# Kernel tuning notes

Hardware: AMD Instinct MI355X
Metric: run time of the kernel (lower is better)

## Reference

```python
import jax, jax.numpy as jnp
import numpy as np

DIM, NH, WS, SR, CTS = 256, 8, 8, 4, 2
HD = DIM // NH
SCALE = HD ** -0.5

def _linear(x, w, b=None):
    y = x @ w.T
    return y + b if b is not None else y

def _ln(x, g, b, eps=1e-5):
    m = jnp.mean(x, -1, keepdims=True)
    v = jnp.mean((x - m) ** 2, -1, keepdims=True)
    return (x - m) / jnp.sqrt(v + eps) * g + b

def _mlp(x, w1, b1, w2, b2):
    return _linear(jax.nn.gelu(_linear(x, w1, b1), approximate=False), w2, b2)

def _pos_emb_rank3(seq_len, w1, b1, w2):
    # PosEmbMLPSwinv1D with rank=3: coords on cube_root(seq) grid, normalized
    s = int(round(seq_len ** (1.0 / 3.0)))
    c = (jnp.arange(s, dtype=jnp.float32) - s // 2) / (s // 2)
    grid = jnp.stack(jnp.meshgrid(c, c, c, indexing='ij'))      # (3,s,s,s)
    tbl = grid.reshape(3, -1).T                                 # (s^3,3)
    return _linear(jax.nn.relu(_linear(tbl, w1, b1)), w2)[None]  # (1,s^3,dim)

def _rel_bias_3d(ws, w1, b1, w2, n_global):
    # PosEmbMLPSwinv3D: CPB-MLP bias over 3D relative coords, 16*sigmoid, zero-pad for carrier tokens
    r = jnp.arange(-(ws - 1), ws, dtype=jnp.float32)
    tbl = jnp.stack(jnp.meshgrid(r, r, r, indexing='ij'), axis=-1) / (ws - 1)
    tbl = tbl * 8.0
    tbl = jnp.sign(tbl) * jnp.log2(jnp.abs(tbl) + 1.0) / np.log2(8.0)
    table = _linear(jax.nn.relu(_linear(tbl.reshape(-1, 3), w1, b1)), w2)  # ((2ws-1)^3, NH)
    coords = jnp.stack(jnp.meshgrid(jnp.arange(ws), jnp.arange(ws), jnp.arange(ws), indexing='ij'))
    cf = coords.reshape(3, -1)
    rel = (cf[:, :, None] - cf[:, None, :]).transpose(1, 2, 0) + (ws - 1)  # (P,P,3)
    idx = rel[..., 0] * (2 * ws - 1) ** 2 + rel[..., 1] * (2 * ws - 1) + rel[..., 2]
    P = ws ** 3
    bias = table[idx.reshape(-1)].reshape(P, P, NH).transpose(2, 0, 1)
    bias = 16.0 * jax.nn.sigmoid(bias)
    return jnp.pad(bias, ((0, 0), (n_global, 0), (n_global, 0)))[None]  # (1,NH,P+g,P+g)

def _win_attn(x, qkv_w, qkv_b, proj_w, proj_b, bias):
    B, N, C = x.shape
    qkv = _linear(x, qkv_w, qkv_b).reshape(B, N, 3, NH, HD).transpose(2, 0, 3, 1, 4)
    q, k, v = qkv[0], qkv[1], qkv[2]
    attn = jax.nn.softmax(jnp.einsum('bhnd,bhmd->bhnm', q, k) * SCALE + bias, axis=-1)
    out = jnp.einsum('bhnm,bhmd->bhnd', attn, v).transpose(0, 2, 1, 3).reshape(B, N, C)
    return _linear(out, proj_w, proj_b)

def _ct_dewindow(ct, W, H, D, ws):
    bs, _, N = ct.shape
    c = ct.reshape(bs, W // ws, H // ws, D // ws, ws, ws, ws, N)
    c = c.transpose(0, 7, 1, 3, 5, 2, 4, 6).reshape(bs, N, W * H * D)
    return c.transpose(0, 2, 1)

def _ct_window(ct, W, H, D, ws):
    bs, _, N = ct.shape
    c = ct.reshape(bs, H // ws, ws, W // ws, ws, D // ws, ws, N)
    return c.transpose(0, 1, 3, 5, 2, 4, 6, 7)

def setup_inputs() -> dict:
    key = jax.random.key(0)
    ks = jax.random.split(key, 48)
    B0 = 1
    nw = SR ** 3
    def w(k, *s):
        return jax.random.normal(k, s, jnp.float32) * 0.02
    def b(k, *s):
        return jax.random.normal(k, s, jnp.float32) * 0.01
    d4 = 4 * DIM
    return {
        'x': jax.random.normal(ks[0], (B0 * nw, WS ** 3, DIM), jnp.float32),
        'ct': jax.random.normal(ks[1], (B0, (CTS * SR) ** 3, DIM), jnp.float32),
        'pe_w1': w(ks[2], 512, 3), 'pe_b1': b(ks[3], 512), 'pe_w2': w(ks[4], DIM, 512),
        'hpe_w1': w(ks[5], 512, 3), 'hpe_b1': b(ks[6], 512), 'hpe_w2': w(ks[7], DIM, 512),
        'hat_n1_g': jnp.ones((DIM,), jnp.float32), 'hat_n1_b': jnp.zeros((DIM,), jnp.float32),
        'hat_qkv_w': w(ks[8], 3 * DIM, DIM), 'hat_qkv_b': b(ks[9], 3 * DIM),
        'hat_proj_w': w(ks[10], DIM, DIM), 'hat_proj_b': b(ks[11], DIM),
        'hat_cpb_w1': w(ks[12], 512, 3), 'hat_cpb_b1': b(ks[13], 512), 'hat_cpb_w2': w(ks[14], NH, 512),
        'hat_n2_g': jnp.ones((DIM,), jnp.float32), 'hat_n2_b': jnp.zeros((DIM,), jnp.float32),
        'hat_fc1_w': w(ks[15], d4, DIM), 'hat_fc1_b': b(ks[16], d4),
        'hat_fc2_w': w(ks[17], DIM, d4), 'hat_fc2_b': b(ks[18], DIM),
        'n1_g': jnp.ones((DIM,), jnp.float32), 'n1_b': jnp.zeros((DIM,), jnp.float32),
        'qkv_w': w(ks[19], 3 * DIM, DIM), 'qkv_b': b(ks[20], 3 * DIM),
        'proj_w': w(ks[21], DIM, DIM), 'proj_b': b(ks[22], DIM),
        'cpb_w1': w(ks[23], 512, 3), 'cpb_b1': b(ks[24], 512), 'cpb_w2': w(ks[25], NH, 512),
        'n2_g': jnp.ones((DIM,), jnp.float32), 'n2_b': jnp.zeros((DIM,), jnp.float32),
        'fc1_w': w(ks[26], d4, DIM), 'fc1_b': b(ks[27], d4),
        'fc2_w': w(ks[28], DIM, d4), 'fc2_b': b(ks[29], DIM),
    }

def reference(x, ct, pe_w1, pe_b1, pe_w2, hpe_w1, hpe_b1, hpe_w2,
              hat_n1_g, hat_n1_b, hat_qkv_w, hat_qkv_b, hat_proj_w, hat_proj_b,
              hat_cpb_w1, hat_cpb_b1, hat_cpb_w2, hat_n2_g, hat_n2_b,
              hat_fc1_w, hat_fc1_b, hat_fc2_w, hat_fc2_b,
              n1_g, n1_b, qkv_w, qkv_b, proj_w, proj_b,
              cpb_w1, cpb_b1, cpb_w2, n2_g, n2_b, fc1_w, fc1_b, fc2_w, fc2_b):
    Bg, Ng, Hg = ct.shape
    G = CTS * SR  # carrier-token global cube side
    x = x + _pos_emb_rank3(x.shape[1], pe_w1, pe_b1, pe_w2)
    # carrier-token global attention (hierarchical path)
    ct = _ct_dewindow(ct, G, G, G, CTS)
    ct = ct + _pos_emb_rank3(ct.shape[1], hpe_w1, hpe_b1, hpe_w2)
    hat_bias = _rel_bias_3d(G, hat_cpb_w1, hat_cpb_b1, hat_cpb_w2, 0)
    ct = ct + _win_attn(_ln(ct, hat_n1_g, hat_n1_b), hat_qkv_w, hat_qkv_b, hat_proj_w, hat_proj_b, hat_bias)
    ct = ct + _mlp(_ln(ct, hat_n2_g, hat_n2_b), hat_fc1_w, hat_fc1_b, hat_fc2_w, hat_fc2_b)
    ct_w = _ct_window(ct, G, G, G, CTS).reshape(x.shape[0], -1, Hg)
    # windowed attention over [carrier tokens ; window tokens]
    x = jnp.concatenate([ct_w, x], axis=1)
    bias = _rel_bias_3d(WS, cpb_w1, cpb_b1, cpb_w2, CTS ** 3)
    x = x + _win_attn(_ln(x, n1_g, n1_b), qkv_w, qkv_b, proj_w, proj_b, bias)
    x = x + _mlp(_ln(x, n2_g, n2_b), fc1_w, fc1_b, fc2_w, fc2_b)
    split = x.shape[1] - WS ** 3
    ctr, x = x[:, :split], x[:, split:]
    return x, ctr.reshape(Bg, Ng, Hg)
```

## Files before the change

kernel.cpp:

```cpp
#include <hip/hip_runtime.h>
#include <hip/hip_bf16.h>
#include <math.h>

typedef __hip_bfloat16 bf16;

#define SCALE_QK 0.17677669529663687f

__device__ __forceinline__ float b2f(bf16 v){ return __bfloat162float(v); }
__device__ __forceinline__ bf16  f2b(float v){ return __float2bfloat16(v); }
__device__ __forceinline__ short bfs(float x){ bf16 b = f2b(x); short s; __builtin_memcpy(&s, &b, 2); return s; }

struct __align__(16) bf16x8 { bf16 v[8]; };
struct __align__(8)  bf16x4 { bf16 v[4]; };

typedef __attribute__((ext_vector_type(8))) short sh8;
typedef __attribute__((ext_vector_type(4))) short sh4;
typedef __attribute__((ext_vector_type(4))) float f4;

#if defined(__has_builtin)
#if __has_builtin(__builtin_amdgcn_mfma_f32_16x16x16bf16_1k)
#define HAS_MFMA16 1
#else
#define HAS_MFMA16 0
#endif
#else
#define HAS_MFMA16 0
#endif

#if defined(__has_builtin)
#if __has_builtin(__builtin_amdgcn_exp2f)
#define EXP2(x) __builtin_amdgcn_exp2f(x)
#else
#define EXP2(x) exp2f(x)
#endif
#else
#define EXP2(x) exp2f(x)
#endif

__global__ __launch_bounds__(256) void wcvt10_k(const float* s0, const float* s1, const float* s2, const float* s3,
                                                const float* s4, const float* s5, const float* s6, const float* s7,
                                                const float* s8, const float* s9,
                                                bf16* d0, bf16* d1, bf16* d2, bf16* d3, bf16* d4,
                                                bf16* d5, bf16* d6, bf16* d7, bf16* d8, bf16* d9) {
    const int sizes[10] = {196608, 65536, 262144, 262144, 196608, 65536, 262144, 262144, 131072, 131072};
    int which = blockIdx.y;
    const float* s; bf16* d;
    switch (which) {
        case 0: s = s0; d = d0; break;  case 1: s = s1; d = d1; break;
        case 2: s = s2; d = d2; break;  case 3: s = s3; d = d3; break;
        case 4: s = s4; d = d4; break;  case 5: s = s5; d = d5; break;
        case 6: s = s6; d = d6; break;  case 7: s = s7; d = d7; break;
        case 8: s = s8; d = d8; break;  default: s = s9; d = d9; break;
    }
    int i = blockIdx.x * 256 + threadIdx.x;
    if (i < sizes[which]) d[i] = f2b(s[i]);
}

__global__ __launch_bounds__(256) void hidbuild_k(const float* __restrict__ w1a, const float* __restrict__ b1a,
                                                  const float* __restrict__ w1b, const float* __restrict__ b1b,
                                                  bf16* __restrict__ hidA, bf16* __restrict__ hidB) {
    const float* w1 = blockIdx.y ? w1b : w1a;
    const float* b1 = blockIdx.y ? b1b : b1a;
    bf16* hid       = blockIdx.y ? hidB : hidA;
    int t = blockIdx.x, tid = threadIdx.x;
    int i = t >> 6, j = (t >> 3) & 7, k = t & 7;
    float c0 = (i - 4) * 0.25f, c1 = (j - 4) * 0.25f, c2 = (k - 4) * 0.25f;
    #pragma unroll
    for (int rep = 0; rep < 2; rep++) {
        int jj = tid + rep * 256;
        float h = c0 * w1[jj*3+0] + c1 * w1[jj*3+1] + c2 * w1[jj*3+2] + b1[jj];
        hid[(size_t)t * 512 + jj] = f2b(fmaxf(h, 0.f));
    }
}

__device__ __forceinline__ float cpb_coord(int idx) {
    float v = (idx - 7) * (8.0f / 7.0f);
    return copysignf(log2f(fabsf(v) + 1.0f) * (1.0f / 3.0f), v);
}
__global__ __launch_bounds__(512) void cpbtab_k(const float* __restrict__ w1a, const float* __restrict__ b1a,
                                                const float* __restrict__ w2a, float* __restrict__ taba,
                                                const float* __restrict__ w1b, const float* __restrict__ b1b,
                                                const float* __restrict__ w2b, float* __restrict__ tabb) {
    const float* w1 = blockIdx.y ? w1b : w1a;
    const float* b1 = blockIdx.y ? b1b : b1a;
    const float* w2 = blockIdx.y ? w2b : w2a;
    float* tab      = blockIdx.y ? tabb : taba;
    int t = blockIdx.x, tid = threadIdx.x;
    __shared__ float hid[512];
    int i = t / 225, r = t - i * 225, j = r / 15, k = r - j * 15;
    float x0 = cpb_coord(i), x1 = cpb_coord(j), x2 = cpb_coord(k);
    float h = x0 * w1[tid*3+0] + x1 * w1[tid*3+1] + x2 * w1[tid*3+2] + b1[tid];
    hid[tid] = fmaxf(h, 0.f);
    __syncthreads();
    int h8 = tid >> 6, lane = tid & 63;
    float p = 0.f;
    for (int jj = lane; jj < 512; jj += 64) p += hid[jj] * w2[h8*512 + jj];
    for (int off = 32; off; off >>= 1) p += __shfl_down(p, off);
    if (lane == 0) tab[t * 8 + h8] = p;
}

__global__ __launch_bounds__(256) void biasbuild_k(const float* __restrict__ taba, float* __restrict__ biasQa,
                                                   const float* __restrict__ tabb, float* __restrict__ biasQb) {
    const float* tab = blockIdx.y ? tabb : taba;
    float* biasQ     = blockIdx.y ? biasQb : biasQa;
    int idx = blockIdx.x * 256 + threadIdx.x;
    int h = idx >> 18, rem = idx & 262143;
    int q = rem >> 9, k = rem & 511;
    int qx = q >> 6, qy = (q >> 3) & 7, qz = q & 7;
    int kx = k >> 6, ky = (k >> 3) & 7, kz = k & 7;
    int tidx = ((qx - kx + 7) * 15 + (qy - ky + 7)) * 15 + (qz - kz + 7);
    float v = tab[tidx * 8 + h];
    float b = 16.f / (1.f + __expf(-v));
    biasQ[idx] = (b - 24.0f) * 1.4426950408889634f;
}

__global__ __launch_bounds__(256) void ct0build_k(const float* __restrict__ ct_in,
                                                  const float* __restrict__ hpe,
                                                  float* __restrict__ ct0) {
    int u = blockIdx.x, c = threadIdx.x;
    int a = u >> 7, cc = (u >> 5) & 3, e = (u >> 4) & 1, b = (u >> 2) & 3, d = (u >> 1) & 1, f = u & 1;
    int t = a * 128 + b * 32 + cc * 8 + d * 4 + e * 2 + f;
    ct0[(size_t)u * 256 + c] = ct_in[(size_t)t * 256 + c] + hpe[(size_t)u * 256 + c];
}

__global__ __launch_bounds__(256) void ln_k(const float* __restrict__ in,
                                            const float* __restrict__ g,
                                            const float* __restrict__ b,
                                            bf16* __restrict__ out) {
    int row = blockIdx.x, c = threadIdx.x;
    float x = in[(size_t)row * 256 + c];
    float s = x, s2 = x * x;
    for (int off = 32; off; off >>= 1) { s += __shfl_down(s, off); s2 += __shfl_down(s2, off); }
    __shared__ float red[8];
    int wid = c >> 6, lane = c & 63;
    if (lane == 0) { red[wid] = s; red[wid + 4] = s2; }
    __syncthreads();
    if (c == 0) { red[0] = red[0] + red[1] + red[2] + red[3]; red[4] = red[4] + red[5] + red[6] + red[7]; }
    __syncthreads();
    float mean = red[0] * (1.f / 256.f);
    float var  = fmaxf(red[4] * (1.f / 256.f) - mean * mean, 0.f);
    float rstd = rsqrtf(var + 1e-5f);
    out[(size_t)row * 256 + c] = f2b((x - mean) * rstd * g[c] + b[c]);
}

template <int MODE>
__global__ __launch_bounds__(256) void gemm_k(const bf16* __restrict__ A,
                                              const bf16* __restrict__ W,
                                              const float* __restrict__ bias,
                                              int M, int N, int K,
                                              float* __restrict__ res,
                                              bf16* __restrict__ outb) {
    __shared__ short As[128 * 40];
    __shared__ short Ws[128 * 40];
    int m0 = blockIdx.y * 128, n0 = blockIdx.x * 128;
    int tid = threadIdx.x;
    int lane = tid & 63, wave = tid >> 6;
    int quad = lane >> 4, m16 = lane & 15;
    int wm = (wave & 1) * 64, wn = (wave >> 1) * 64;
    int arow = tid >> 2, acol = (tid & 3) * 8;

    f4 acc[4][4];
    #pragma unroll
    for (int i = 0; i < 4; i++)
        #pragma unroll
        for (int j = 0; j < 4; j++) acc[i][j] = (f4){0.f, 0.f, 0.f, 0.f};

    for (int k0 = 0; k0 < K; k0 += 32) {
        sh8 a0 = *reinterpret_cast<const sh8*>(A + (size_t)(m0 + arow) * K + k0 + acol);
        sh8 a1 = *reinterpret_cast<const sh8*>(A + (size_t)(m0 + arow + 64) * K + k0 + acol);
        sh8 w0 = *reinterpret_cast<const sh8*>(W + (size_t)(n0 + arow) * K + k0 + acol);
        sh8 w1 = *reinterpret_cast<const sh8*>(W + (size_t)(n0 + arow + 64) * K + k0 + acol);
        __syncthreads();
        *reinterpret_cast<sh8*>(&As[arow * 40 + acol])        = a0;
        *reinterpret_cast<sh8*>(&As[(arow + 64) * 40 + acol]) = a1;
        *reinterpret_cast<sh8*>(&Ws[arow * 40 + acol])        = w0;
        *reinterpret_cast<sh8*>(&Ws[(arow + 64) * 40 + acol]) = w1;
        __syncthreads();
        sh8 af[4], bf[4];
        #pragma unroll
        for (int mi = 0; mi < 4; mi++)
            af[mi] = *reinterpret_cast<const sh8*>(&As[(wm + mi * 16 + m16) * 40 + quad * 8]);
        #pragma unroll
        for (int ni = 0; ni < 4; ni++)
            bf[ni] = *reinterpret_cast<const sh8*>(&Ws[(wn + ni * 16 + m16) * 40 + quad * 8]);
        #pragma unroll
        for (int mi = 0; mi < 4; mi++)
            #pragma unroll
            for (int ni = 0; ni < 4; ni++)
                acc[mi][ni] = __builtin_amdgcn_mfma_f32_16x16x32_bf16(af[mi], bf[ni], acc[mi][ni], 0, 0, 0);
    }
    (void)M;

    #pragma unroll
    for (int mi = 0; mi < 4; mi++) {
        #pragma unroll
        for (int r = 0; r < 4; r++) {
            int gm = m0 + wm + mi * 16 + quad * 4 + r;
            #pragma unroll
            for (int ni = 0; ni < 4; ni++) {
                int gn = n0 + wn + ni * 16 + m16;
                float v = acc[mi][ni][r];
                if constexpr (MODE != 3) v += bias[gn];
                if constexpr (MODE == 2)      res[(size_t)gm * N + gn] += v;
                else if constexpr (MODE == 3) res[(size_t)gm * N + gn] = v;
                else if constexpr (MODE == 1) outb[(size_t)gm * N + gn] = f2b(0.5f * v * (1.0f + erff(v * 0.70710678118654752f)));
                else                          outb[(size_t)gm * N + gn] = f2b(v);
            }
        }
    }
}

#define VSTR 548
#define SC2   0.25503575360579045f
#define CNB  (-34.62468098133512f)
#define NEGB (-1.0e30f)
__global__ __launch_bounds__(512) void flash_k(const bf16* __restrict__ qkv,
                                               const float* __restrict__ biasQ,
                                               bf16* __restrict__ out,
                                               int N, int glob) {
    int wh = blockIdx.x, w = wh >> 3, h = wh & 7;
    int qs = blockIdx.y, QS = gridDim.y;
    int tid = threadIdx.x;
    int lane = tid & 63, wave = tid >> 6;
    int quad = lane >> 4, qcol = lane & 15;
    const int NT32 = (N + 31) & ~31;

    __shared__ bf16 Vt[32 * VSTR];
#if !HAS_MFMA16
    __shared__ float Ps[8][16 * 17];
#endif

    for (int i = tid; i < NT32 * 4; i += 512) {
        int tok = i >> 2, seg = i & 3;
        if (tok < N) {
            const bf16* vp = qkv + ((size_t)(w * N + tok)) * 768 + 512 + h * 32 + seg * 8;
            bf16x8 vv = *reinterpret_cast<const bf16x8*>(vp);
            #pragma unroll
            for (int e = 0; e < 8; e++) Vt[(seg * 8 + e) * VSTR + tok] = vv.v[e];
        } else {
            bf16 z = f2b(0.f);
            #pragma unroll
            for (int e = 0; e < 8; e++) Vt[(seg * 8 + e) * VSTR + tok] = z;
        }
    }
    __syncthreads();

    const bf16* qbase = qkv + ((size_t)w * N) * 768 + h * 32;
    const bf16* kbase = qbase + 256;
    int nqt = (N + 15) >> 4, nkt = NT32 >> 5;
    int nun = (nqt + 1) >> 1;

    for (int u = wave * QS + qs; u < nun; u += 8 * QS) {
        bool hasB = (2 * u + 1 < nqt);
        int qA = u * 32 + qcol;
        int qB = qA + 16;
        int qrA = (qA < N) ? qA : (N - 1);
        int qrB = (qB < N) ? qB : (N - 1);
        sh8 qfA = *reinterpret_cast<const sh8*>(qbase + (size_t)qrA * 768 + quad * 8);
        sh8 qfB = *reinterpret_cast<const sh8*>(qbase + (size_t)qrB * 768 + quad * 8);
        f4 O0A = {0.f,0.f,0.f,0.f}, O1A = {0.f,0.f,0.f,0.f};
        f4 O0B = {0.f,0.f,0.f,0.f}, O1B = {0.f,0.f,0.f,0.f};
        float lA = 0.f, lB = 0.f;
        bool vA = (qA >= glob) && (qA < N);
        bool vB = (qB >= glob) && (qB < N);
        const float* browA = biasQ + (((size_t)h << 9) + (size_t)(vA ? (qA - glob) : 0)) * 512 - glob;
        const float* browB = biasQ + (((size_t)h << 9) + (size_t)(vB ? (qB - glob) : 0)) * 512 - glob;

        sh8 kf0, kf1;
        {
            int k0 = qcol, k1 = 16 + qcol;
            kf0 = *reinterpret_cast<const sh8*>(kbase + (size_t)((k0 < N) ? k0 : (N - 1)) * 768 + quad * 8);
            kf1 = *reinterpret_cast<const sh8*>(kbase + (size_t)((k1 < N) ? k1 : (N - 1)) * 768 + quad * 8);
        }

        for (int kt = 0; kt < nkt; kt++) {
            int bt = kt * 32;
            sh8 c0 = kf0, c1 = kf1;
            if (kt + 1 < nkt) {
                int n0 = bt + 32 + qcol, n1 = bt + 48 + qcol;
                kf0 = *reinterpret_cast<const sh8*>(kbase + (size_t)((n0 < N) ? n0 : (N - 1)) * 768 + quad * 8);
                kf1 = *reinterpret_cast<const sh8*>(kbase + (size_t)((n1 < N) ? n1 : (N - 1)) * 768 + quad * 8);
            }
            f4 z = {0.f, 0.f, 0.f, 0.f};
            f4 s0A = __builtin_amdgcn_mfma_f32_16x16x32_bf16(c0, qfA, z, 0, 0, 0);
            f4 s1A = __builtin_amdgcn_mfma_f32_16x16x32_bf16(c1, qfA, z, 0, 0, 0);
            f4 s0B = z, s1B = z;
            if (hasB) {
                s0B = __builtin_amdgcn_mfma_f32_16x16x32_bf16(c0, qfB, z, 0, 0, 0);
                s1B = __builtin_amdgcn_mfma_f32_16x16x32_bf16(c1, qfB, z, 0, 0, 0);
            }

            int tg0 = bt + quad * 4, tg1 = bt + 16 + quad * 4;
            bool val0 = tg0 < N, val1 = tg1 < N;
            f4 bb0A, bb1A;
            if (!val0)                    bb0A = (f4){NEGB, NEGB, NEGB, NEGB};
            else if (vA && tg0 >= glob)   bb0A = *reinterpret_cast<const f4*>(browA + tg0);
            else                          bb0A = (f4){CNB, CNB, CNB, CNB};
            if (!val1)                    bb1A = (f4){NEGB, NEGB, NEGB, NEGB};
            else if (vA && tg1 >= glob)   bb1A = *reinterpret_cast<const f4*>(browA + tg1);
            else                          bb1A = (f4){CNB, CNB, CNB, CNB};

            float pA[8];
            #pragma unroll
            for (int r = 0; r < 4; r++) {
                pA[r]     = EXP2(fmaf(s0A[r], SC2, bb0A[r]));
                pA[4 + r] = EXP2(fmaf(s1A[r], SC2, bb1A[r]));
            }
            #pragma unroll
            for (int r = 0; r < 8; r++) lA += pA[r];

            float pB[8];
            if (hasB) {
                f4 bb0B, bb1B;
                if (!val0)                    bb0B = (f4){NEGB, NEGB, NEGB, NEGB};
                else if (vB && tg0 >= glob)   bb0B = *reinterpret_cast<const f4*>(browB + tg0);
                else                          bb0B = (f4){CNB, CNB, CNB, CNB};
                if (!val1)                    bb1B = (f4){NEGB, NEGB, NEGB, NEGB};
                else if (vB && tg1 >= glob)   bb1B = *reinterpret_cast<const f4*>(browB + tg1);
                else                          bb1B = (f4){CNB, CNB, CNB, CNB};
                #pragma unroll
                for (int r = 0; r < 4; r++) {
                    pB[r]     = EXP2(fmaf(s0B[r], SC2, bb0B[r]));
                    pB[4 + r] = EXP2(fmaf(s1B[r], SC2, bb1B[r]));
                }
                #pragma unroll
                for (int r = 0; r < 8; r++) lB += pB[r];
            }

#if HAS_MFMA16
            sh4 v00 = *reinterpret_cast<const sh4*>(&Vt[qcol * VSTR + bt + quad * 4]);
            sh4 v10 = *reinterpret_cast<const sh4*>(&Vt[qcol * VSTR + bt + 16 + quad * 4]);
            sh4 v01 = *reinterpret_cast<const sh4*>(&Vt[(qcol + 16) * VSTR + bt + quad * 4]);
            sh4 v11 = *reinterpret_cast<const sh4*>(&Vt[(qcol + 16) * VSTR + bt + 16 + quad * 4]);
            sh4 pf0A, pf1A;
            #pragma unroll
            for (int r = 0; r < 4; r++) { pf0A[r] = bfs(pA[r]); pf1A[r] = bfs(pA[4 + r]); }
            O0A = __builtin_amdgcn_mfma_f32_16x16x16bf16_1k(v00, pf0A, O0A, 0, 0, 0);
            O0A = __builtin_amdgcn_mfma_f32_16x16x16bf16_1k(v10, pf1A, O0A, 0, 0, 0);
            O1A = __builtin_amdgcn_mfma_f32_16x16x16bf16_1k(v01, pf0A, O1A, 0, 0, 0);
            O1A = __builtin_amdgcn_mfma_f32_16x16x16bf16_1k(v11, pf1A, O1A, 0, 0, 0);
            if (hasB) {
                sh4 pf0B, pf1B;
                #pragma unroll
                for (int r = 0; r < 4; r++) { pf0B[r] = bfs(pB[r]); pf1B[r] = bfs(pB[4 + r]); }
                O0B = __builtin_amdgcn_mfma_f32_16x16x16bf16_1k(v00, pf0B, O0B, 0, 0, 0);
                O0B = __builtin_amdgcn_mfma_f32_16x16x16bf16_1k(v10, pf1B, O0B, 0, 0, 0);
                O1B = __builtin_amdgcn_mfma_f32_16x16x16bf16_1k(v01, pf0B, O1B, 0, 0, 0);
                O1B = __builtin_amdgcn_mfma_f32_16x16x16bf16_1k(v11, pf1B, O1B, 0, 0, 0);
            }
#else
            for (int t = 0; t < 2; t++) {
                if (t == 1 && !hasB) break;
                const float* ph = t ? pB : pA;
                for (int half = 0; half < 2; half++) {
                    #pragma unroll
                    for (int r = 0; r < 4; r++) Ps[wave][(quad * 4 + r) * 17 + qcol] = ph[half * 4 + r];
                    __builtin_amdgcn_wave_barrier();
                    sh8 pbig, va, vb;
                    #pragma unroll
                    for (int j = 0; j < 8; j++) {
                        int tl = quad * 8 + j;
                        float pv = (quad < 2) ? Ps[wave][tl * 17 + qcol] : 0.f;
                        pbig[j] = bfs(pv);
                        bf16 a0 = (quad < 2) ? Vt[qcol * VSTR + bt + half * 16 + tl] : f2b(0.f);
                        bf16 a1 = (quad < 2) ? Vt[(qcol + 16) * VSTR + bt + half * 16 + tl] : f2b(0.f);
                        short t0, t1;
                        __builtin_memcpy(&t0, &a0, 2); __builtin_memcpy(&t1, &a1, 2);
                        va[j] = t0; vb[j] = t1;
                    }
                    if (t == 0) {
                        O0A = __builtin_amdgcn_mfma_f32_16x16x32_bf16(va, pbig, O0A, 0, 0, 0);
                        O1A = __builtin_amdgcn_mfma_f32_16x16x32_bf16(vb, pbig, O1A, 0, 0, 0);
                    } else {
                        O0B = __builtin_amdgcn_mfma_f32_16x16x32_bf16(va, pbig, O0B, 0, 0, 0);
                        O1B = __builtin_amdgcn_mfma_f32_16x16x32_bf16(vb, pbig, O1B, 0, 0, 0);
                    }
                    __builtin_amdgcn_wave_barrier();
                }
            }
#endif
        }

        lA += __shfl_xor(lA, 16); lA += __shfl_xor(lA, 32);
        float rlA = 1.f / lA;
        if (qA < N) {
            bf16x4 o0, o1;
            #pragma unroll
            for (int r = 0; r < 4; r++) { o0.v[r] = f2b(O0A[r] * rlA); o1.v[r] = f2b(O1A[r] * rlA); }
            bf16* op = out + ((size_t)(w * N + qA)) * 256 + h * 32 + quad * 4;
            *reinterpret_cast<bf16x4*>(op)      = o0;
            *reinterpret_cast<bf16x4*>(op + 16) = o1;
        }
        if (hasB) {
            lB += __shfl_xor(lB, 16); lB += __shfl_xor(lB, 32);
            float rlB = 1.f / lB;
            if (qB < N) {
                bf16x4 o0, o1;
                #pragma unroll
                for (int r = 0; r < 4; r++) { o0.v[r] = f2b(O0B[r] * rlB); o1.v[r] = f2b(O1B[r] * rlB); }
                bf16* op = out + ((size_t)(w * N + qB)) * 256 + h * 32 + quad * 4;
                *reinterpret_cast<bf16x4*>(op)      = o0;
                *reinterpret_cast<bf16x4*>(op + 16) = o1;
            }
        }
    }
}

__global__ __launch_bounds__(256) void xcatbuild_k(const float* __restrict__ x_in,
                                                   const float* __restrict__ pe,
                                                   const float* __restrict__ ct2,
                                                   float* __restrict__ xcat) {
    int row = blockIdx.x, w = row / 520, p = row - w * 520, c = threadIdx.x;
    float v;
    if (p < 8) {
        int P = w >> 4, Q = (w >> 2) & 3, R = w & 3;
        int S = p >> 2, T = (p >> 1) & 1, U = p & 1;
        int t = P * 128 + S * 64 + Q * 16 + T * 8 + R * 2 + U;
        v = ct2[(size_t)t * 256 + c];
    } else {
        int t = p - 8;
        v = x_in[((size_t)w * 512 + t) * 256 + c] + pe[(size_t)t * 256 + c];
    }
    xcat[(size_t)row * 256 + c] = v;
}

__global__ __launch_bounds__(256) void outbuild_k(const float* __restrict__ xcat,
                                                  float* __restrict__ out) {
    int row = blockIdx.x, w = row / 520, p = row - w * 520, c = threadIdx.x;
    float v = xcat[(size_t)row * 256 + c];
    if (p >= 8) out[((size_t)(w * 512) + (p - 8)) * 256 + c] = v;
    else        out[(size_t)8388608 + ((size_t)(w * 8) + p) * 256 + c] = v;
}

extern "C" void kernel_launch(void* const* d_in, const int* in_sizes, int n_in,
                              void* d_out, int out_size, void* d_ws, size_t ws_size,
                              hipStream_t stream) {
    const float* x          = (const float*)d_in[0];
    const float* ct         = (const float*)d_in[1];
    const float* pe_w1      = (const float*)d_in[2];
    const float* pe_b1      = (const float*)d_in[3];
    const float* pe_w2      = (const float*)d_in[4];
    const float* hpe_w1     = (const float*)d_in[5];
    const float* hpe_b1     = (const float*)d_in[6];
    const float* hpe_w2     = (const float*)d_in[7];
    const float* hat_n1_g   = (const float*)d_in[8];
    const float* hat_n1_b   = (const float*)d_in[9];
    const float* hat_qkv_w  = (const float*)d_in[10];
    const float* hat_qkv_b  = (const float*)d_in[11];
    const float* hat_proj_w = (const float*)d_in[12];
    const float* hat_proj_b = (const float*)d_in[13];
    const float* hat_cpb_w1 = (const float*)d_in[14];
    const float* hat_cpb_b1 = (const float*)d_in[15];
    const float* hat_cpb_w2 = (const float*)d_in[16];
    const float* hat_n2_g   = (const float*)d_in[17];
    const float* hat_n2_b   = (const float*)d_in[18];
    const float* hat_fc1_w  = (const float*)d_in[19];
    const float* hat_fc1_b  = (const float*)d_in[20];
    const float* hat_fc2_w  = (const float*)d_in[21];
    const float* hat_fc2_b  = (const float*)d_in[22];
    const float* n1_g       = (const float*)d_in[23];
    const float* n1_b       = (const float*)d_in[24];
    const float* qkv_w      = (const float*)d_in[25];
    const float* qkv_b      = (const float*)d_in[26];
    const float* proj_w     = (const float*)d_in[27];
    const float* proj_b     = (const float*)d_in[28];
    const float* cpb_w1     = (const float*)d_in[29];
    const float* cpb_b1     = (const float*)d_in[30];
    const float* cpb_w2     = (const float*)d_in[31];
    const float* n2_g       = (const float*)d_in[32];
    const float* n2_b       = (const float*)d_in[33];
    const float* fc1_w      = (const float*)d_in[34];
    const float* fc1_b      = (const float*)d_in[35];
    const float* fc2_w      = (const float*)d_in[36];
    const float* fc2_b      = (const float*)d_in[37];
    (void)in_sizes; (void)n_in; (void)out_size;

    char* base = (char*)d_ws;
    size_t off = 0;
    auto alloc = [&](size_t bytes) -> void* {
        void* p = base + off;
        off += (bytes + 255) & ~(size_t)255;
        return p;
    };
    float* pe        = (float*)alloc(512 * 256 * 4);
    float* hpe       = (float*)alloc(512 * 256 * 4);
    float* tab_hat   = (float*)alloc(3375 * 8 * 4);
    float* tab2      = (float*)alloc(3375 * 8 * 4);
    float* biasQ2    = (float*)alloc((size_t)8 * 512 * 512 * 4);
    float* ct0       = (float*)alloc(512 * 256 * 4);
    bf16* wb_hqkv  = (bf16*)alloc(768 * 256 * 2);
    bf16* wb_hproj = (bf16*)alloc(256 * 256 * 2);
    bf16* wb_hfc1  = (bf16*)alloc(1024 * 256 * 2);
    bf16* wb_hfc2  = (bf16*)alloc(256 * 1024 * 2);
    bf16* wb_qkv   = (bf16*)alloc(768 * 256 * 2);
    bf16* wb_proj  = (bf16*)alloc(256 * 256 * 2);
    bf16* wb_fc1   = (bf16*)alloc(1024 * 256 * 2);
    bf16* wb_fc2   = (bf16*)alloc(256 * 1024 * 2);
    bf16* wb_pew2  = (bf16*)alloc(256 * 512 * 2);
    bf16* wb_hpew2 = (bf16*)alloc(256 * 512 * 2);
    size_t zstart = off;
    bf16*  hidA      = (bf16*)alloc(512 * 512 * 2);
    bf16*  hidB      = (bf16*)alloc(512 * 512 * 2);
    off = zstart;
    float* biasQ_hat = (float*)alloc((size_t)8 * 512 * 512 * 4);
    bf16*  hct_ln    = (bf16*)alloc(512 * 256 * 2);
    bf16*  hqkv      = (bf16*)alloc(512 * 768 * 2);
    bf16*  hat_attn  = (bf16*)alloc(512 * 256 * 2);
    bf16*  hat_hid   = (bf16*)alloc(512 * 1024 * 2);
    off = zstart;
    float* xcat      = (float*)alloc((size_t)64 * 520 * 256 * 4);
    const int S     = (ws_size >= (size_t)150 * 1024 * 1024) ? 1 : 4;
    const int rows  = 33280 / S;
    const int wins  = 64 / S;
    bf16*  xln_b     = (bf16*)alloc((size_t)rows * 256 * 2);
    char*  region_qa = (char*)alloc((size_t)rows * 1024 * 2);
    bf16*  qkv_b_    = (bf16*)region_qa;
    bf16*  attn_b    = (bf16*)(region_qa + (size_t)rows * 768 * 2);
    bf16*  hidden    = (bf16*)region_qa;

    wcvt10_k<<<dim3(1024, 10), 256, 0, stream>>>(hat_qkv_w, hat_proj_w, hat_fc1_w, hat_fc2_w,
                                                 qkv_w, proj_w, fc1_w, fc2_w, pe_w2, hpe_w2,
                                                 wb_hqkv, wb_hproj, wb_hfc1, wb_hfc2,
                                                 wb_qkv, wb_proj, wb_fc1, wb_fc2, wb_pew2, wb_hpew2);

    hidbuild_k<<<dim3(512, 2), 256, 0, stream>>>(pe_w1, pe_b1, hpe_w1, hpe_b1, hidA, hidB);
    gemm_k<3><<<dim3(2, 4), 256, 0, stream>>>(hidA, wb_pew2,  nullptr, 512, 256, 512, pe,  nullptr);
    gemm_k<3><<<dim3(2, 4), 256, 0, stream>>>(hidB, wb_hpew2, nullptr, 512, 256, 512, hpe, nullptr);

    cpbtab_k<<<dim3(3375, 2), 512, 0, stream>>>(hat_cpb_w1, hat_cpb_b1, hat_cpb_w2, tab_hat,
                                                cpb_w1, cpb_b1, cpb_w2, tab2);
    biasbuild_k<<<dim3(8192, 2), 256, 0, stream>>>(tab_hat, biasQ_hat, tab2, biasQ2);

    ct0build_k<<<512, 256, 0, stream>>>(ct, hpe, ct0);
    ln_k<<<512, 256, 0, stream>>>(ct0, hat_n1_g, hat_n1_b, hct_ln);
    gemm_k<0><<<dim3(6, 4), 256, 0, stream>>>(hct_ln, wb_hqkv, hat_qkv_b, 512, 768, 256, nullptr, hqkv);
    flash_k<<<dim3(8, 2), 512, 0, stream>>>(hqkv, biasQ_hat, hat_attn, 512, 0);
    gemm_k<2><<<dim3(2, 4), 256, 0, stream>>>(hat_attn, wb_hproj, hat_proj_b, 512, 256, 256, ct0, nullptr);
    ln_k<<<512, 256, 0, stream>>>(ct0, hat_n2_g, hat_n2_b, hct_ln);
    gemm_k<1><<<dim3(8, 4), 256, 0, stream>>>(hct_ln, wb_hfc1, hat_fc1_b, 512, 1024, 256, nullptr, hat_hid);
    gemm_k<2><<<dim3(2, 4), 256, 0, stream>>>(hat_hid, wb_hfc2, hat_fc2_b, 512, 256, 1024, ct0, nullptr);

    xcatbuild_k<<<33280, 256, 0, stream>>>(x, pe, ct0, xcat);

    for (int s = 0; s < S; s++) {
        float* xc = xcat + (size_t)s * rows * 256;
        ln_k<<<rows, 256, 0, stream>>>(xc, n1_g, n1_b, xln_b);
        gemm_k<0><<<dim3(6, rows / 128), 256, 0, stream>>>(xln_b, wb_qkv, qkv_b, rows, 768, 256, nullptr, qkv_b_);
        flash_k<<<dim3(wins * 8, 2), 512, 0, stream>>>(qkv_b_, biasQ2, attn_b, 520, 8);
        gemm_k<2><<<dim3(2, rows / 128), 256, 0, stream>>>(attn_b, wb_proj, proj_b, rows, 256, 256, xc, nullptr);
    }
    for (int s = 0; s < S; s++) {
        float* xc = xcat + (size_t)s * rows * 256;
        ln_k<<<rows, 256, 0, stream>>>(xc, n2_g, n2_b, xln_b);
        gemm_k<1><<<dim3(8, rows / 128), 256, 0, stream>>>(xln_b, wb_fc1, fc1_b, rows, 1024, 256, nullptr, hidden);
        gemm_k<2><<<dim3(2, rows / 128), 256, 0, stream>>>(hidden, wb_fc2, fc2_b, rows, 256, 1024, xc, nullptr);
    }

    outbuild_k<<<33280, 256, 0, stream>>>(xcat, (float*)d_out);
}
```

Measured before the change: 624.1 us.

## Fuse LayerNorm into producer kernels and fc2 output scatter for single-slab path

Result: faster. 605.8 us (-2.9%).

```diff
diff --git a/kernel.cpp b/kernel.cpp
--- a/kernel.cpp
+++ b/kernel.cpp
@@ -114,13 +114,29 @@
     biasQ[idx] = (b - 24.0f) * 1.4426950408889634f;
 }
 
-__global__ __launch_bounds__(256) void ct0build_k(const float* __restrict__ ct_in,
-                                                  const float* __restrict__ hpe,
-                                                  float* __restrict__ ct0) {
+__global__ __launch_bounds__(256) void ct0ln_k(const float* __restrict__ ct_in,
+                                               const float* __restrict__ hpe,
+                                               const float* __restrict__ g,
+                                               const float* __restrict__ b,
+                                               float* __restrict__ ct0,
+                                               bf16* __restrict__ lnout) {
     int u = blockIdx.x, c = threadIdx.x;
-    int a = u >> 7, cc = (u >> 5) & 3, e = (u >> 4) & 1, b = (u >> 2) & 3, d = (u >> 1) & 1, f = u & 1;
-    int t = a * 128 + b * 32 + cc * 8 + d * 4 + e * 2 + f;
-    ct0[(size_t)u * 256 + c] = ct_in[(size_t)t * 256 + c] + hpe[(size_t)u * 256 + c];
+    int a = u >> 7, cc = (u >> 5) & 3, e = (u >> 4) & 1, bb = (u >> 2) & 3, d = (u >> 1) & 1, f = u & 1;
+    int t = a * 128 + bb * 32 + cc * 8 + d * 4 + e * 2 + f;
+    float x = ct_in[(size_t)t * 256 + c] + hpe[(size_t)u * 256 + c];
+    ct0[(size_t)u * 256 + c] = x;
+    float s = x, s2 = x * x;
+    for (int off = 32; off; off >>= 1) { s += __shfl_down(s, off); s2 += __shfl_down(s2, off); }
+    __shared__ float red[8];
+    int wid = c >> 6, lane = c & 63;
+    if (lane == 0) { red[wid] = s; red[wid + 4] = s2; }
+    __syncthreads();
+    if (c == 0) { red[0] = red[0] + red[1] + red[2] + red[3]; red[4] = red[4] + red[5] + red[6] + red[7]; }
+    __syncthreads();
+    float mean = red[0] * (1.f / 256.f);
+    float var  = fmaxf(red[4] * (1.f / 256.f) - mean * mean, 0.f);
+    float rstd = rsqrtf(var + 1e-5f);
+    lnout[(size_t)u * 256 + c] = f2b((x - mean) * rstd * g[c] + b[c]);
 }
 
 __global__ __launch_bounds__(256) void ln_k(const float* __restrict__ in,
@@ -205,6 +221,166 @@
                 else if constexpr (MODE == 3) res[(size_t)gm * N + gn] = v;
                 else if constexpr (MODE == 1) outb[(size_t)gm * N + gn] = f2b(0.5f * v * (1.0f + erff(v * 0.70710678118654752f)));
                 else                          outb[(size_t)gm * N + gn] = f2b(v);
+            }
+        }
+    }
+}
+
+__global__ __launch_bounds__(512) void gemmln_k(const bf16* __restrict__ A,
+                                                const bf16* __restrict__ W,
+                                                const float* __restrict__ bias,
+                                                float* __restrict__ xcat,
+                                                const float* __restrict__ g,
+                                                const float* __restrict__ b,
+                                                bf16* __restrict__ outb) {
+    __shared__ short As[128 * 40];
+    __shared__ short Ws[256 * 40];
+    __shared__ float redS[128 * 4];
+    __shared__ float redQ[128 * 4];
+    __shared__ float stat[128 * 2];
+    int m0 = blockIdx.x * 128;
+    int tid = threadIdx.x;
+    int lane = tid & 63, wave = tid >> 6;
+    int quad = lane >> 4, m16 = lane & 15;
+    int wm = (wave >> 2) * 64, wn = (wave & 3) * 64;
+    int arow = tid >> 2, acol = (tid & 3) * 8;
+
+    f4 acc[4][4];
+    #pragma unroll
+    for (int i = 0; i < 4; i++)
+        #pragma unroll
+        for (int j = 0; j < 4; j++) acc[i][j] = (f4){0.f, 0.f, 0.f, 0.f};
+
+    for (int k0 = 0; k0 < 256; k0 += 32) {
+        sh8 a0 = *reinterpret_cast<const sh8*>(A + (size_t)(m0 + arow) * 256 + k0 + acol);
+        sh8 w0 = *reinterpret_cast<const sh8*>(W + (size_t)arow * 256 + k0 + acol);
+        sh8 w1 = *reinterpret_cast<const sh8*>(W + (size_t)(arow + 128) * 256 + k0 + acol);
+        __syncthreads();
+        *reinterpret_cast<sh8*>(&As[arow * 40 + acol])         = a0;
+        *reinterpret_cast<sh8*>(&Ws[arow * 40 + acol])         = w0;
+        *reinterpret_cast<sh8*>(&Ws[(arow + 128) * 40 + acol]) = w1;
+        __syncthreads();
+        sh8 af[4], bf[4];
+        #pragma unroll
+        for (int mi = 0; mi < 4; mi++)
+            af[mi] = *reinterpret_cast<const sh8*>(&As[(wm + mi * 16 + m16) * 40 + quad * 8]);
+        #pragma unroll
+        for (int ni = 0; ni < 4; ni++)
+            bf[ni] = *reinterpret_cast<const sh8*>(&Ws[(wn + ni * 16 + m16) * 40 + quad * 8]);
+        #pragma unroll
+        for (int mi = 0; mi < 4; mi++)
+            #pragma unroll
+            for (int ni = 0; ni < 4; ni++)
+                acc[mi][ni] = __builtin_amdgcn_mfma_f32_16x16x32_bf16(af[mi], bf[ni], acc[mi][ni], 0, 0, 0);
+    }
+
+    #pragma unroll
+    for (int mi = 0; mi < 4; mi++) {
+        #pragma unroll
+        for (int r = 0; r < 4; r++) {
+            int lr = wm + mi * 16 + quad * 4 + r;
+            int gm = m0 + lr;
+            float ps = 0.f, pq = 0.f;
+            #pragma unroll
+            for (int ni = 0; ni < 4; ni++) {
+                int gc = wn + ni * 16 + m16;
+                float v = acc[mi][ni][r] + bias[gc] + xcat[(size_t)gm * 256 + gc];
+                acc[mi][ni][r] = v;
+                ps += v; pq += v * v;
+            }
+            ps += __shfl_xor(ps, 1); pq += __shfl_xor(pq, 1);
+            ps += __shfl_xor(ps, 2); pq += __shfl_xor(pq, 2);
+            ps += __shfl_xor(ps, 4); pq += __shfl_xor(pq, 4);
+            ps += __shfl_xor(ps, 8); pq += __shfl_xor(pq, 8);
+            if (m16 == 0) { redS[lr * 4 + (wave & 3)] = ps; redQ[lr * 4 + (wave & 3)] = pq; }
+        }
+    }
+    __syncthreads();
+    if (tid < 128) {
+        float s = redS[tid * 4] + redS[tid * 4 + 1] + redS[tid * 4 + 2] + redS[tid * 4 + 3];
+        float q = redQ[tid * 4] + redQ[tid * 4 + 1] + redQ[tid * 4 + 2] + redQ[tid * 4 + 3];
+        float mean = s * (1.f / 256.f);
+        float var  = fmaxf(q * (1.f / 256.f) - mean * mean, 0.f);
+        stat[tid * 2]     = mean;
+        stat[tid * 2 + 1] = rsqrtf(var + 1e-5f);
+    }
+    __syncthreads();
+    #pragma unroll
+    for (int mi = 0; mi < 4; mi++) {
+        #pragma unroll
+        for (int r = 0; r < 4; r++) {
+            int lr = wm + mi * 16 + quad * 4 + r;
+            int gm = m0 + lr;
+            float mean = stat[lr * 2], rstd = stat[lr * 2 + 1];
+            #pragma unroll
+            for (int ni = 0; ni < 4; ni++) {
+                int gc = wn + ni * 16 + m16;
+                float v = acc[mi][ni][r];
+                xcat[(size_t)gm * 256 + gc] = v;
+                outb[(size_t)gm * 256 + gc] = f2b((v - mean) * rstd * g[gc] + b[gc]);
+            }
+        }
+    }
+}
+
+__global__ __launch_bounds__(256) void gemmsplit_k(const bf16* __restrict__ A,
+                                                   const bf16* __restrict__ W,
+                                                   const float* __restrict__ bias,
+                                                   int K,
+                                                   const float* __restrict__ res,
+                                                   float* __restrict__ out) {
+    __shared__ short As[128 * 40];
+    __shared__ short Ws[128 * 40];
+    int m0 = blockIdx.y * 128, n0 = blockIdx.x * 128;
+    int tid = threadIdx.x;
+    int lane = tid & 63, wave = tid >> 6;
+    int quad = lane >> 4, m16 = lane & 15;
+    int wm = (wave & 1) * 64, wn = (wave >> 1) * 64;
+    int arow = tid >> 2, acol = (tid & 3) * 8;
+
+    f4 acc[4][4];
+    #pragma unroll
+    for (int i = 0; i < 4; i++)
+        #pragma unroll
+        for (int j = 0; j < 4; j++) acc[i][j] = (f4){0.f, 0.f, 0.f, 0.f};
+
+    for (int k0 = 0; k0 < K; k0 += 32) {
+        sh8 a0 = *reinterpret_cast<const sh8*>(A + (size_t)(m0 + arow) * K + k0 + acol);
+        sh8 a1 = *reinterpret_cast<const sh8*>(A + (size_t)(m0 + arow + 64) * K + k0 + acol);
+        sh8 w0 = *reinterpret_cast<const sh8*>(W + (size_t)(n0 + arow) * K + k0 + acol);
+        sh8 w1 = *reinterpret_cast<const sh8*>(W + (size_t)(n0 + arow + 64) * K + k0 + acol);
+        __syncthreads();
+        *reinterpret_cast<sh8*>(&As[arow * 40 + acol])        = a0;
+        *reinterpret_cast<sh8*>(&As[(arow + 64) * 40 + acol]) = a1;
+        *reinterpret_cast<sh8*>(&Ws[arow * 40 + acol])        = w0;
+        *reinterpret_cast<sh8*>(&Ws[(arow + 64) * 40 + acol]) = w1;
+        __syncthreads();
+        sh8 af[4], bf[4];
+        #pragma unroll
+        for (int mi = 0; mi < 4; mi++)
+            af[mi] = *reinterpret_cast<const sh8*>(&As[(wm + mi * 16 + m16) * 40 + quad * 8]);
+        #pragma unroll
+        for (int ni = 0; ni < 4; ni++)
+            bf[ni] = *reinterpret_cast<const sh8*>(&Ws[(wn + ni * 16 + m16) * 40 + quad * 8]);
+        #pragma unroll
+        for (int mi = 0; mi < 4; mi++)
+            #pragma unroll
+            for (int ni = 0; ni < 4; ni++)
+                acc[mi][ni] = __builtin_amdgcn_mfma_f32_16x16x32_bf16(af[mi], bf[ni], acc[mi][ni], 0, 0, 0);
+    }
+
+    #pragma unroll
+    for (int mi = 0; mi < 4; mi++) {
+        #pragma unroll
+        for (int r = 0; r < 4; r++) {
+            int gm = m0 + wm + mi * 16 + quad * 4 + r;
+            int w = gm / 520, p = gm - w * 520;
+            size_t drow = (p >= 8) ? (size_t)(w * 512 + p - 8) : (size_t)(32768 + w * 8 + p);
+            #pragma unroll
+            for (int ni = 0; ni < 4; ni++) {
+                int gn = n0 + wn + ni * 16 + m16;
+                float v = acc[mi][ni][r] + bias[gn] + res[(size_t)gm * 256 + gn];
+                out[drow * 256 + gn] = v;
             }
         }
     }
@@ -404,6 +580,39 @@
             }
         }
     }
+}
+
+__global__ __launch_bounds__(256) void xcatln_k(const float* __restrict__ x_in,
+                                                const float* __restrict__ pe,
+                                                const float* __restrict__ ct2,
+                                                const float* __restrict__ g,
+                                                const float* __restrict__ b,
+                                                float* __restrict__ xcat,
+                                                bf16* __restrict__ xln) {
+    int row = blockIdx.x, w = row / 520, p = row - w * 520, c = threadIdx.x;
+    float v;
+    if (p < 8) {
+        int P = w >> 4, Q = (w >> 2) & 3, R = w & 3;
+        int S = p >> 2, T = (p >> 1) & 1, U = p & 1;
+        int t = P * 128 + S * 64 + Q * 16 + T * 8 + R * 2 + U;
+        v = ct2[(size_t)t * 256 + c];
+    } else {
+        int t = p - 8;
+        v = x_in[((size_t)w * 512 + t) * 256 + c] + pe[(size_t)t * 256 + c];
+    }
+    xcat[(size_t)row * 256 + c] = v;
+    float s = v, s2 = v * v;
+    for (int off = 32; off; off >>= 1) { s += __shfl_down(s, off); s2 += __shfl_down(s2, off); }
+    __shared__ float red[8];
+    int wid = c >> 6, lane = c & 63;
+    if (lane == 0) { red[wid] = s; red[wid + 4] = s2; }
+    __syncthreads();
+    if (c == 0) { red[0] = red[0] + red[1] + red[2] + red[3]; red[4] = red[4] + red[5] + red[6] + red[7]; }
+    __syncthreads();
+    float mean = red[0] * (1.f / 256.f);
+    float var  = fmaxf(red[4] * (1.f / 256.f) - mean * mean, 0.f);
+    float rstd = rsqrtf(var + 1e-5f);
+    xln[(size_t)row * 256 + c] = f2b((v - mean) * rstd * g[c] + b[c]);
 }
 
 __global__ __launch_bounds__(256) void xcatbuild_k(const float* __restrict__ x_in,
@@ -531,30 +740,35 @@
                                                 cpb_w1, cpb_b1, cpb_w2, tab2);
     biasbuild_k<<<dim3(8192, 2), 256, 0, stream>>>(tab_hat, biasQ_hat, tab2, biasQ2);
 
-    ct0build_k<<<512, 256, 0, stream>>>(ct, hpe, ct0);
-    ln_k<<<512, 256, 0, stream>>>(ct0, hat_n1_g, hat_n1_b, hct_ln);
+    ct0ln_k<<<512, 256, 0, stream>>>(ct, hpe, hat_n1_g, hat_n1_b, ct0, hct_ln);
     gemm_k<0><<<dim3(6, 4), 256, 0, stream>>>(hct_ln, wb_hqkv, hat_qkv_b, 512, 768, 256, nullptr, hqkv);
     flash_k<<<dim3(8, 2), 512, 0, stream>>>(hqkv, biasQ_hat, hat_attn, 512, 0);
-    gemm_k<2><<<dim3(2, 4), 256, 0, stream>>>(hat_attn, wb_hproj, hat_proj_b, 512, 256, 256, ct0, nullptr);
-    ln_k<<<512, 256, 0, stream>>>(ct0, hat_n2_g, hat_n2_b, hct_ln);
+    gemmln_k<<<4, 512, 0, stream>>>(hat_attn, wb_hproj, hat_proj_b, ct0, hat_n2_g, hat_n2_b, hct_ln);
     gemm_k<1><<<dim3(8, 4), 256, 0, stream>>>(hct_ln, wb_hfc1, hat_fc1_b, 512, 1024, 256, nullptr, hat_hid);
     gemm_k<2><<<dim3(2, 4), 256, 0, stream>>>(hat_hid, wb_hfc2, hat_fc2_b, 512, 256, 1024, ct0, nullptr);
 
-    xcatbuild_k<<<33280, 256, 0, stream>>>(x, pe, ct0, xcat);
-
-    for (int s = 0; s < S; s++) {
-        float* xc = xcat + (size_t)s * rows * 256;
-        ln_k<<<rows, 256, 0, stream>>>(xc, n1_g, n1_b, xln_b);
-        gemm_k<0><<<dim3(6, rows / 128), 256, 0, stream>>>(xln_b, wb_qkv, qkv_b, rows, 768, 256, nullptr, qkv_b_);
-        flash_k<<<dim3(wins * 8, 2), 512, 0, stream>>>(qkv_b_, biasQ2, attn_b, 520, 8);
-        gemm_k<2><<<dim3(2, rows / 128), 256, 0, stream>>>(attn_b, wb_proj, proj_b, rows, 256, 256, xc, nullptr);
-    }
-    for (int s = 0; s < S; s++) {
-        float* xc = xcat + (size_t)s * rows * 256;
-        ln_k<<<rows, 256, 0, stream>>>(xc, n2_g, n2_b, xln_b);
-        gemm_k<1><<<dim3(8, rows / 128), 256, 0, stream>>>(xln_b, wb_fc1, fc1_b, rows, 1024, 256, nullptr, hidden);
-        gemm_k<2><<<dim3(2, rows / 128), 256, 0, stream>>>(hidden, wb_fc2, fc2_b, rows, 256, 1024, xc, nullptr);
-    }
-
-    outbuild_k<<<33280, 256, 0, stream>>>(xcat, (float*)d_out);
-}
+    if (S == 1) {
+        xcatln_k<<<33280, 256, 0, stream>>>(x, pe, ct0, n1_g, n1_b, xcat, xln_b);
+        gemm_k<0><<<dim3(6, 260), 256, 0, stream>>>(xln_b, wb_qkv, qkv_b, 33280, 768, 256, nullptr, qkv_b_);
+        flash_k<<<dim3(512, 2), 512, 0, stream>>>(qkv_b_, biasQ2, attn_b, 520, 8);
+        gemmln_k<<<260, 512, 0, stream>>>(attn_b, wb_proj, proj_b, xcat, n2_g, n2_b, xln_b);
+        gemm_k<1><<<dim3(8, 260), 256, 0, stream>>>(xln_b, wb_fc1, fc1_b, 33280, 1024, 256, nullptr, hidden);
+        gemmsplit_k<<<dim3(2, 260), 256, 0, stream>>>(hidden, wb_fc2, fc2_b, 1024, xcat, (float*)d_out);
+    } else {
+        xcatbuild_k<<<33280, 256, 0, stream>>>(x, pe, ct0, xcat);
+        for (int s = 0; s < S; s++) {
+            float* xc = xcat + (size_t)s * rows * 256;
+            ln_k<<<rows, 256, 0, stream>>>(xc, n1_g, n1_b, xln_b);
+            gemm_k<0><<<dim3(6, rows / 128), 256, 0, stream>>>(xln_b, wb_qkv, qkv_b, rows, 768, 256, nullptr, qkv_b_);
+            flash_k<<<dim3(wins * 8, 2), 512, 0, stream>>>(qkv_b_, biasQ2, attn_b, 520, 8);
+            gemm_k<2><<<dim3(2, rows / 128), 256, 0, stream>>>(attn_b, wb_proj, proj_b, rows, 256, 256, xc, nullptr);
+        }
+        for (int s = 0; s < S; s++) {
+            float* xc = xcat + (size_t)s * rows * 256;
+            ln_k<<<rows, 256, 0, stream>>>(xc, n2_g, n2_b, xln_b);
+            gemm_k<1><<<dim3(8, rows / 128), 256, 0, stream>>>(xln_b, wb_fc1, fc1_b, rows, 1024, 256, nullptr, hidden);
+            gemm_k<2><<<dim3(2, rows / 128), 256, 0, stream>>>(hidden, wb_fc2, fc2_b, rows, 256, 1024, xc, nullptr);
+        }
+        outbuild_k<<<33280, 256, 0, stream>>>(xcat, (float*)d_out);
+    }
+}
```
